# Optimization experiments

Measured on AMD Instinct MI355X. Metric: run time of the kernel, lower is better.

The kernel has to match this reference:

```python
import jax, jax.numpy as jnp
import numpy as np

C = 256
C8 = C // 8
B, D, H, W = 2, 16, 64, 64


def setup_inputs() -> dict:
    key = jax.random.key(0)
    ks = jax.random.split(key, 8)
    s = 0.05
    return {
        "x1": jax.random.normal(ks[0], (B, C, D, H, W), dtype=jnp.float32),
        "x2": jax.random.normal(ks[1], (B, C, D, H, W), dtype=jnp.float32),
        "Wq": jax.random.normal(ks[2], (C8, C), dtype=jnp.float32) * s,
        "bq": jax.random.normal(ks[3], (C8,), dtype=jnp.float32) * s,
        "Wk": jax.random.normal(ks[4], (C8, C), dtype=jnp.float32) * s,
        "bk": jax.random.normal(ks[5], (C8,), dtype=jnp.float32) * s,
        "Wv": jax.random.normal(ks[6], (C, C), dtype=jnp.float32) * s,
        "bv": jax.random.normal(ks[7], (C,), dtype=jnp.float32) * s,
    }


def _conv1x1(x, Wt, b):
    # 1x1x1 Conv3d == channel-mixing linear: x [B,Cin,D,H,W], Wt [Cout,Cin]
    return jnp.einsum('bcdhw,oc->bodhw', x, Wt) + b[None, :, None, None, None]


def reference(x1, x2, Wq, bq, Wk, bk, Wv, bv):
    q = _conv1x1(x1, Wq, bq)   # [B,C8,D,H,W]
    k = _conv1x1(x2, Wk, bk)   # [B,C8,D,H,W]
    v = _conv1x1(x2, Wv, bv)   # [B,C, D,H,W]
    # Non-softmax bilinear attention over the W axis, batched over (b,d,h)
    attn = jnp.einsum('bcdhx,bcdhy->bdhxy', q, k)        # [B,D,H,W,W]
    out = jnp.einsum('bdhxy,bcdhy->bcdhx', attn, v)      # [B,C,D,H,W]
    return out
```

## Files before the change

kernel.cpp:

```cpp
#include <hip/hip_runtime.h>

#define NB   2
#define ND   16
#define NH   64
#define DHW  65536
#define HW   4096
#define CDHW 16777216

typedef __attribute__((ext_vector_type(4))) float f32x4;
typedef __attribute__((ext_vector_type(8))) short bf16x8;
typedef unsigned short ushort_t;

#define MFMA16(a, b, c) __builtin_amdgcn_mfma_f32_16x16x32_bf16((a), (b), (c), 0, 0, 0)

#define WS_WQH 0
#define WS_WQL 8192
#define WS_WKH 16384
#define WS_WKL 24576
#define WS_WVH 32768
#define WS_WVL 98304
#define WS_WEIGHT_USHORTS 163840
#define WS_AH  (WS_WEIGHT_USHORTS)
#define WS_AL  (WS_AH + 8388608)
#define WS_FULL_BYTES ((size_t)(WS_WEIGHT_USHORTS + 16777216) * 2)

__device__ __forceinline__ void split_val(float f, short& h, short& l) {
  unsigned int u = __builtin_bit_cast(unsigned int, f);
  h = (short)(unsigned short)(u >> 16);
  float fh = __builtin_bit_cast(float, u & 0xffff0000u);
  float r = f - fh;
  l = (short)(unsigned short)(__builtin_bit_cast(unsigned int, r) >> 16);
}

__device__ __forceinline__ void load_split8(const float* __restrict__ p, bf16x8& h8, bf16x8& l8) {
  float4 a = *(const float4*)p;
  float4 b = *(const float4*)(p + 4);
  float f[8] = {a.x, a.y, a.z, a.w, b.x, b.y, b.z, b.w};
#pragma unroll
  for (int j = 0; j < 8; ++j) {
    short hh, ll;
    split_val(f[j], hh, ll);
    h8[j] = hh; l8[j] = ll;
  }
}

__device__ __forceinline__ int swzb(int row, int colb) {
  return row * 128 + (((colb) & ~15) ^ ((row & 7) << 4)) + ((colb) & 15);
}

__global__ void prep_w(const float* __restrict__ Wq, const float* __restrict__ Wk,
                       const float* __restrict__ Wv, ushort_t* __restrict__ ws) {
  int idx = blockIdx.x * 256 + threadIdx.x;
  const float* src; int off; ushort_t *H, *L;
  if (idx < 8192)       { src = Wq; off = idx;         H = ws + WS_WQH; L = ws + WS_WQL; }
  else if (idx < 16384) { src = Wk; off = idx - 8192;  H = ws + WS_WKH; L = ws + WS_WKL; }
  else if (idx < 81920) { src = Wv; off = idx - 16384; H = ws + WS_WVH; L = ws + WS_WVL; }
  else return;
  short h, l;
  split_val(src[off], h, l);
  H[off] = (ushort_t)h;
  L[off] = (ushort_t)l;
}

__global__ __launch_bounds__(256, 2) void qk_kernel(
    const float* __restrict__ x1, const float* __restrict__ x2,
    const float* __restrict__ bq, const float* __restrict__ bk,
    ushort_t* __restrict__ ws)
{
  __shared__ char qsmem[32768];
  const int tid  = threadIdx.x;
  const int lane = tid & 63;
  const int wv   = tid >> 6;
  const int l15  = lane & 15;
  const int g    = lane >> 4;

  const int grp = blockIdx.x * 4 + wv;
  const int b   = grp >> 10;
  const int rem = grp & 1023;
  const int d   = rem >> 6;
  const int h   = rem & 63;
  const size_t base = (size_t)b * CDHW + (size_t)d * HW + (size_t)h * 64;
  const float* x1p = x1 + base;
  const float* x2p = x2 + base;

  float* buf = (float*)(qsmem + wv * 8192);

  const ushort_t* WqH = ws + WS_WQH;
  const ushort_t* WqL = ws + WS_WQL;
  const ushort_t* WkH = ws + WS_WKH;
  const ushort_t* WkL = ws + WS_WKL;

  f32x4 qacc[2][4], kacc[2][4];
#pragma unroll
  for (int mt = 0; mt < 2; ++mt) {
    int r0 = mt * 16 + 4 * g;
    f32x4 bqv = (f32x4){bq[r0], bq[r0 + 1], bq[r0 + 2], bq[r0 + 3]};
    f32x4 bkv = (f32x4){bk[r0], bk[r0 + 1], bk[r0 + 2], bk[r0 + 3]};
#pragma unroll
    for (int nt = 0; nt < 4; ++nt) { qacc[mt][nt] = bqv; kacc[mt][nt] = bkv; }
  }

  const int rrow = (lane >> 4);
  const int rcol = (lane & 15) * 4;

  float4 rfA[8], rfB[8];
  auto loadc = [&](float4* rf, int i) {
    const float* src = (i < 8 ? x1p : x2p) + (size_t)(32 * (i & 7)) * DHW;
#pragma unroll
    for (int k = 0; k < 8; ++k)
      rf[k] = *(const float4*)(src + (size_t)(4 * k + rrow) * DHW + rcol);
  };
  auto writec = [&](const float4* rf) {
#pragma unroll
    for (int k = 0; k < 8; ++k)
      *(float4*)&buf[(4 * k + rrow) * 64 + rcol] = rf[k];
  };
  auto compute = [&](int i, f32x4 (&acc)[2][4], const ushort_t* Wh, const ushort_t* Wl) {
    const int kg0 = 32 * (i & 7) + 8 * g;
    bf16x8 wh0 = *(const bf16x8*)&Wh[(size_t)(l15) * 256 + kg0];
    bf16x8 wl0 = *(const bf16x8*)&Wl[(size_t)(l15) * 256 + kg0];
    bf16x8 wh1 = *(const bf16x8*)&Wh[(size_t)(16 + l15) * 256 + kg0];
    bf16x8 wl1 = *(const bf16x8*)&Wl[(size_t)(16 + l15) * 256 + kg0];
    bf16x8 bh[4], bl[4];
#pragma unroll
    for (int nt = 0; nt < 4; ++nt) {
#pragma unroll
      for (int j = 0; j < 8; ++j) {
        float f = buf[(8 * g + j) * 64 + nt * 16 + l15];
        short hh, ll;
        split_val(f, hh, ll);
        bh[nt][j] = hh; bl[nt][j] = ll;
      }
    }
#pragma unroll
    for (int nt = 0; nt < 4; ++nt) {
      acc[0][nt] = MFMA16(wh0, bh[nt], acc[0][nt]);
      acc[0][nt] = MFMA16(wh0, bl[nt], acc[0][nt]);
      acc[0][nt] = MFMA16(wl0, bh[nt], acc[0][nt]);
      acc[1][nt] = MFMA16(wh1, bh[nt], acc[1][nt]);
      acc[1][nt] = MFMA16(wh1, bl[nt], acc[1][nt]);
      acc[1][nt] = MFMA16(wl1, bh[nt], acc[1][nt]);
    }
  };

  loadc(rfA, 0);
#pragma unroll
  for (int i2 = 0; i2 < 8; ++i2) {
    const int i0 = 2 * i2, i1 = 2 * i2 + 1;
    loadc(rfB, i1);
    writec(rfA);
    if (i0 < 8) compute(i0, qacc, WqH, WqL); else compute(i0, kacc, WkH, WkL);
    if (i1 + 1 < 16) loadc(rfA, i1 + 1);
    writec(rfB);
    if (i1 < 8) compute(i1, qacc, WqH, WqL); else compute(i1, kacc, WkH, WkL);
  }

  ushort_t* ex = (ushort_t*)buf;
#pragma unroll
  for (int mt = 0; mt < 2; ++mt)
#pragma unroll
    for (int nt = 0; nt < 4; ++nt)
#pragma unroll
      for (int r = 0; r < 4; ++r) {
        short hh, ll;
        split_val(qacc[mt][nt][r], hh, ll);
        int x = nt * 16 + l15;
        ex[x * 32 + mt * 16 + 4 * g + r]        = (ushort_t)hh;
        ex[2048 + x * 32 + mt * 16 + 4 * g + r] = (ushort_t)ll;
      }
  bf16x8 qh8[4], ql8[4];
#pragma unroll
  for (int mt = 0; mt < 4; ++mt) {
    qh8[mt] = *(const bf16x8*)&ex[(mt * 16 + l15) * 32 + 8 * g];
    ql8[mt] = *(const bf16x8*)&ex[2048 + (mt * 16 + l15) * 32 + 8 * g];
  }
#pragma unroll
  for (int mt = 0; mt < 2; ++mt)
#pragma unroll
    for (int nt = 0; nt < 4; ++nt)
#pragma unroll
      for (int r = 0; r < 4; ++r) {
        short hh, ll;
        split_val(kacc[mt][nt][r], hh, ll);
        int y = nt * 16 + l15;
        ex[y * 32 + mt * 16 + 4 * g + r]        = (ushort_t)hh;
        ex[2048 + y * 32 + mt * 16 + 4 * g + r] = (ushort_t)ll;
      }
  bf16x8 kh8[4], kl8[4];
#pragma unroll
  for (int nt = 0; nt < 4; ++nt) {
    kh8[nt] = *(const bf16x8*)&ex[(nt * 16 + l15) * 32 + 8 * g];
    kl8[nt] = *(const bf16x8*)&ex[2048 + (nt * 16 + l15) * 32 + 8 * g];
  }
  f32x4 aacc[4][4];
#pragma unroll
  for (int mt = 0; mt < 4; ++mt)
#pragma unroll
    for (int nt = 0; nt < 4; ++nt) {
      f32x4 a = (f32x4){0.f, 0.f, 0.f, 0.f};
      a = MFMA16(qh8[mt], kh8[nt], a);
      a = MFMA16(qh8[mt], kl8[nt], a);
      a = MFMA16(ql8[mt], kh8[nt], a);
      aacc[mt][nt] = a;
    }
  ushort_t* Ah = ws + WS_AH + (size_t)grp * 4096;
  ushort_t* Al = ws + WS_AL + (size_t)grp * 4096;
#pragma unroll
  for (int mt = 0; mt < 4; ++mt)
#pragma unroll
    for (int nt = 0; nt < 4; ++nt)
#pragma unroll
      for (int r = 0; r < 4; ++r) {
        short hh, ll;
        split_val(aacc[mt][nt][r], hh, ll);
        int x = mt * 16 + 4 * g + r, y = nt * 16 + l15;
        Ah[x * 64 + y] = (ushort_t)hh;
        Al[x * 64 + y] = (ushort_t)ll;
      }
}

#define B_OFF_XTH  0
#define B_OFF_XTL  8192
#define B_OFF_AH   16384
#define B_OFF_AL   24576
#define B_OFF_XLIN 32768
#define B_SMEM     49152

__global__ __launch_bounds__(256, 3) void xattn_v3(
    const float* __restrict__ x2, const float* __restrict__ bv,
    const ushort_t* __restrict__ wsp, float* __restrict__ out)
{
  __shared__ char smem[B_SMEM];
  char*  XthB = smem + B_OFF_XTH;
  char*  XtlB = smem + B_OFF_XTL;
  char*  AhL  = smem + B_OFF_AH;
  char*  AlL  = smem + B_OFF_AL;
  float* Xlin = (float*)(smem + B_OFF_XLIN);

  const int tid  = threadIdx.x;
  const int lane = tid & 63;
  const int wv   = tid >> 6;
  const int l15  = lane & 15;
  const int g    = lane >> 4;

  const int bid   = blockIdx.x;
  const int grp   = bid >> 1;
  const int chalf = bid & 1;
  const int cbase = chalf * 128;
  const int b   = grp >> 10;
  const int rem = grp & 1023;
  const int d   = rem >> 6;
  const int h   = rem & 63;
  const size_t base = (size_t)b * CDHW + (size_t)d * HW + (size_t)h * 64;
  const float* x2p = x2 + base;

  const ushort_t* WvH = wsp + WS_WVH;
  const ushort_t* WvL = wsp + WS_WVL;
  const ushort_t* AhW = wsp + WS_AH + (size_t)grp * 4096;
  const ushort_t* AlW = wsp + WS_AL + (size_t)grp * 4096;

  float4 pf[4];
  auto issue_pf = [&](const float* __restrict__ src) {
#pragma unroll
    for (int i = 0; i < 4; ++i) {
      int ch = 16 * wv + g + 4 * i;
      pf[i] = *(const float4*)(src + (size_t)ch * DHW + 4 * l15);
    }
  };
  auto write_xlin = [&]() {
#pragma unroll
    for (int i = 0; i < 4; ++i) {
      int ch = 16 * wv + g + 4 * i;
      *(float4*)&Xlin[ch * 64 + 4 * l15] = pf[i];
    }
  };
  auto passB = [&]() {
#pragma unroll
    for (int bb = 0; bb < 2; ++bb) {
      int c0 = 16 * wv + 8 * bb;
      bf16x8 h8, l8;
#pragma unroll
      for (int j = 0; j < 8; ++j) {
        float f = Xlin[(c0 + j) * 64 + lane];
        short hh, ll;
        split_val(f, hh, ll);
        h8[j] = hh; l8[j] = ll;
      }
      *(bf16x8*)(XthB + swzb(lane, c0 * 2)) = h8;
      *(bf16x8*)(XtlB + swzb(lane, c0 * 2)) = l8;
    }
  };
  auto ldsx = [&](const char* B, int row, int ko) -> bf16x8 {
    return *(const bf16x8*)(B + swzb(row, ko * 2));
  };

  f32x4 vacc[2][4];
#pragma unroll
  for (int mt = 0; mt < 2; ++mt) {
    int r0 = cbase + 32 * wv + mt * 16 + 4 * g;
    f32x4 bb = (f32x4){bv[r0], bv[r0 + 1], bv[r0 + 2], bv[r0 + 3]};
#pragma unroll
    for (int nt = 0; nt < 4; ++nt) vacc[mt][nt] = bb;
  }

  issue_pf(x2p);
  {
#pragma unroll
    for (int rr = 0; rr < 2; ++rr) {
      int idx = tid + rr * 256;
      int row = idx >> 3;
      int seg = idx & 7;
      bf16x8 vh = *(const bf16x8*)&AhW[row * 64 + seg * 8];
      bf16x8 vl = *(const bf16x8*)&AlW[row * 64 + seg * 8];
      *(bf16x8*)(AhL + swzb(row, seg * 16)) = vh;
      *(bf16x8*)(AlL + swzb(row, seg * 16)) = vl;
    }
  }
  write_xlin();
  __syncthreads();

  for (int t = 0; t < 4; ++t) {
    bf16x8 w_h[2][2], w_l[2][2];
#pragma unroll
    for (int ks = 0; ks < 2; ++ks) {
      const int kg = t * 64 + ks * 32 + 8 * g;
#pragma unroll
      for (int mt = 0; mt < 2; ++mt) {
        w_h[ks][mt] = *(const bf16x8*)&WvH[(size_t)(cbase + 32 * wv + mt * 16 + l15) * 256 + kg];
        w_l[ks][mt] = *(const bf16x8*)&WvL[(size_t)(cbase + 32 * wv + mt * 16 + l15) * 256 + kg];
      }
    }
    passB();
    __syncthreads();
    if (t < 3) issue_pf(x2p + (size_t)(t + 1) * 64 * DHW);
#pragma unroll
    for (int ks = 0; ks < 2; ++ks) {
      const int ko = ks * 32 + 8 * g;
      bf16x8 xh[4], xl[4];
#pragma unroll
      for (int nt = 0; nt < 4; ++nt) {
        xh[nt] = ldsx(XthB, nt * 16 + l15, ko);
        xl[nt] = ldsx(XtlB, nt * 16 + l15, ko);
      }
      __builtin_amdgcn_s_setprio(1);
#pragma unroll
      for (int mt = 0; mt < 2; ++mt) {
#pragma unroll
        for (int nt = 0; nt < 4; ++nt) {
          vacc[mt][nt] = MFMA16(w_h[ks][mt], xh[nt], vacc[mt][nt]);
          vacc[mt][nt] = MFMA16(w_h[ks][mt], xl[nt], vacc[mt][nt]);
          vacc[mt][nt] = MFMA16(w_l[ks][mt], xh[nt], vacc[mt][nt]);
        }
      }
      __builtin_amdgcn_s_setprio(0);
    }
    if (t < 3) write_xlin();
    __syncthreads();
  }

  {
    char* VhB = smem + B_OFF_XLIN + wv * 4096;
    char* VlB = VhB + 2048;
#pragma unroll
    for (int mt = 0; mt < 2; ++mt) {
#pragma unroll
      for (int nt = 0; nt < 4; ++nt)
#pragma unroll
        for (int r = 0; r < 4; ++r) {
          short hh, ll;
          split_val(vacc[mt][nt][r], hh, ll);
          int colb = (nt * 16 + l15) * 2;
          *(ushort_t*)(VhB + swzb(4 * g + r, colb)) = (ushort_t)hh;
          *(ushort_t*)(VlB + swzb(4 * g + r, colb)) = (ushort_t)ll;
        }
      f32x4 oacc[4];
#pragma unroll
      for (int nt = 0; nt < 4; ++nt) oacc[nt] = (f32x4){0.f, 0.f, 0.f, 0.f};
      __builtin_amdgcn_s_setprio(1);
#pragma unroll
      for (int ys = 0; ys < 2; ++ys) {
        const int yo = ys * 32 + 8 * g;
        bf16x8 vh8 = *(const bf16x8*)(VhB + swzb(l15, yo * 2));
        bf16x8 vl8 = *(const bf16x8*)(VlB + swzb(l15, yo * 2));
#pragma unroll
        for (int nt = 0; nt < 4; ++nt) {
          bf16x8 ah8 = ldsx(AhL, nt * 16 + l15, yo);
          bf16x8 al8 = ldsx(AlL, nt * 16 + l15, yo);
          oacc[nt] = MFMA16(vh8, ah8, oacc[nt]);
          oacc[nt] = MFMA16(vh8, al8, oacc[nt]);
          oacc[nt] = MFMA16(vl8, ah8, oacc[nt]);
        }
      }
      __builtin_amdgcn_s_setprio(0);
#pragma unroll
      for (int nt = 0; nt < 4; ++nt)
#pragma unroll
        for (int r = 0; r < 4; ++r)
          out[base + (size_t)(cbase + 32 * wv + mt * 16 + 4 * g + r) * DHW + nt * 16 + l15] = oacc[nt][r];
    }
  }
}

#define XT_LD 72
#define QK_LD 40
#define A_LD  72
#define VB_LD 72
#define F_OFF_XTH 0
#define F_OFF_XTL 9216
#define F_OFF_R2  18432
#define F_OFF_KH  18432
#define F_OFF_KL  23552
#define F_OFF_AH  0
#define F_OFF_AL  9216
#define F_OFF_QH  36864
#define F_OFF_QL  41984
#define F_SMEM 47104

__global__ __launch_bounds__(256, 3) void xattn_fallback(
    const float* __restrict__ x1, const float* __restrict__ x2,
    const float* __restrict__ Wq, const float* __restrict__ bq,
    const float* __restrict__ Wk, const float* __restrict__ bk,
    const float* __restrict__ Wv, const float* __restrict__ bv,
    float* __restrict__ out)
{
  __shared__ char smem[F_SMEM];
  ushort_t* Xth  = (ushort_t*)(smem + F_OFF_XTH);
  ushort_t* Xtl  = (ushort_t*)(smem + F_OFF_XTL);
  float*    Xlin = (float*)(smem + F_OFF_R2);
  ushort_t* Kh   = (ushort_t*)(smem + F_OFF_KH);
  ushort_t* Kl   = (ushort_t*)(smem + F_OFF_KL);
  ushort_t* Vb   = (ushort_t*)(smem + F_OFF_R2);
  ushort_t* Ah   = (ushort_t*)(smem + F_OFF_AH);
  ushort_t* Al   = (ushort_t*)(smem + F_OFF_AL);
  ushort_t* Qh   = (ushort_t*)(smem + F_OFF_QH);
  ushort_t* Ql   = (ushort_t*)(smem + F_OFF_QL);

  const int tid  = threadIdx.x;
  const int lane = tid & 63;
  const int wv   = tid >> 6;
  const int l15  = lane & 15;
  const int g    = lane >> 4;

  const int grp = blockIdx.x;
  const int b   = grp >> 10;
  const int rem = grp & 1023;
  const int d   = rem >> 6;
  const int h   = rem & 63;
  const size_t base = (size_t)b * CDHW + (size_t)d * HW + (size_t)h * 64;

  auto passA = [&](const float* __restrict__ src) {
#pragma unroll
    for (int i = 0; i < 4; ++i) {
      int ch = 16 * wv + (lane >> 4) + 4 * i;
      int c4 = (lane & 15) << 2;
      float4 v = *(const float4*)(src + (size_t)ch * DHW + c4);
      *(float4*)&Xlin[ch * 66 + c4] = v;
    }
  };
  auto passB = [&]() {
#pragma unroll
    for (int bb = 0; bb < 2; ++bb) {
      int c0 = 16 * wv + 8 * bb;
      bf16x8 h8, l8;
#pragma unroll
      for (int j = 0; j < 8; ++j) {
        float f = Xlin[(c0 + j) * 66 + lane];
        short hh, ll;
        split_val(f, hh, ll);
        h8[j] = hh; l8[j] = ll;
      }
      *(bf16x8*)&Xth[lane * XT_LD + c0] = h8;
      *(bf16x8*)&Xtl[lane * XT_LD + c0] = l8;
    }
  };

  {
    f32x4 qacc[2];
#pragma unroll
    for (int mt = 0; mt < 2; ++mt) {
      int r0 = mt * 16 + 4 * g;
      qacc[mt] = (f32x4){bq[r0], bq[r0 + 1], bq[r0 + 2], bq[r0 + 3]};
    }
    const float* x1p = x1 + base;
    for (int t = 0; t < 4; ++t) {
      passA(x1p + (size_t)t * 64 * DHW);
      __syncthreads();
      passB();
      __syncthreads();
#pragma unroll
      for (int ks = 0; ks < 2; ++ks) {
        const int ko = ks * 32 + 8 * g;
        const int kg = t * 64 + ko;
        bf16x8 bh = *(const bf16x8*)&Xth[(16 * wv + l15) * XT_LD + ko];
        bf16x8 bl = *(const bf16x8*)&Xtl[(16 * wv + l15) * XT_LD + ko];
#pragma unroll
        for (int mt = 0; mt < 2; ++mt) {
          bf16x8 wh, wl;
          load_split8(Wq + (size_t)(mt * 16 + l15) * 256 + kg, wh, wl);
          qacc[mt] = MFMA16(wh, bh, qacc[mt]);
          qacc[mt] = MFMA16(wh, bl, qacc[mt]);
          qacc[mt] = MFMA16(wl, bh, qacc[mt]);
        }
      }
      __syncthreads();
    }
    const int x = 16 * wv + l15;
#pragma unroll
    for (int mt = 0; mt < 2; ++mt)
#pragma unroll
      for (int r = 0; r < 4; ++r) {
        short hh, ll;
        split_val(qacc[mt][r], hh, ll);
        Qh[x * QK_LD + mt * 16 + 4 * g + r] = (ushort_t)hh;
        Ql[x * QK_LD + mt * 16 + 4 * g + r] = (ushort_t)ll;
      }
  }

  f32x4 vacc[4][4];
  {
    f32x4 kacc[2];
#pragma unroll
    for (int mt = 0; mt < 2; ++mt) {
      int r0 = mt * 16 + 4 * g;
      kacc[mt] = (f32x4){bk[r0], bk[r0 + 1], bk[r0 + 2], bk[r0 + 3]};
    }
#pragma unroll
    for (int mt = 0; mt < 4; ++mt) {
      int r0 = 64 * wv + mt * 16 + 4 * g;
      f32x4 bb = (f32x4){bv[r0], bv[r0 + 1], bv[r0 + 2], bv[r0 + 3]};
#pragma unroll
      for (int nt = 0; nt < 4; ++nt) vacc[mt][nt] = bb;
    }
    const float* x2p = x2 + base;
    for (int t = 0; t < 4; ++t) {
      passA(x2p + (size_t)t * 64 * DHW);
      __syncthreads();
      passB();
      __syncthreads();
#pragma unroll
      for (int ks = 0; ks < 2; ++ks) {
        const int ko = ks * 32 + 8 * g;
        const int kg = t * 64 + ko;
        bf16x8 xh[4], xl[4];
#pragma unroll
        for (int nt = 0; nt < 4; ++nt) {
          xh[nt] = *(const bf16x8*)&Xth[(nt * 16 + l15) * XT_LD + ko];
          xl[nt] = *(const bf16x8*)&Xtl[(nt * 16 + l15) * XT_LD + ko];
        }
        {
          bf16x8 bh = *(const bf16x8*)&Xth[(16 * wv + l15) * XT_LD + ko];
          bf16x8 bl = *(const bf16x8*)&Xtl[(16 * wv + l15) * XT_LD + ko];
#pragma unroll
          for (int mt = 0; mt < 2; ++mt) {
            bf16x8 wh, wl;
            load_split8(Wk + (size_t)(mt * 16 + l15) * 256 + kg, wh, wl);
            kacc[mt] = MFMA16(wh, bh, kacc[mt]);
            kacc[mt] = MFMA16(wh, bl, kacc[mt]);
            kacc[mt] = MFMA16(wl, bh, kacc[mt]);
          }
        }
#pragma unroll
        for (int mt = 0; mt < 4; ++mt) {
          bf16x8 wh, wl;
          load_split8(Wv + (size_t)(64 * wv + mt * 16 + l15) * 256 + kg, wh, wl);
#pragma unroll
          for (int nt = 0; nt < 4; ++nt) {
            vacc[mt][nt] = MFMA16(wh, xh[nt], vacc[mt][nt]);
            vacc[mt][nt] = MFMA16(wh, xl[nt], vacc[mt][nt]);
            vacc[mt][nt] = MFMA16(wl, xh[nt], vacc[mt][nt]);
          }
        }
      }
      __syncthreads();
    }
    const int y = 16 * wv + l15;
#pragma unroll
    for (int mt = 0; mt < 2; ++mt)
#pragma unroll
      for (int r = 0; r < 4; ++r) {
        short hh, ll;
        split_val(kacc[mt][r], hh, ll);
        Kh[y * QK_LD + mt * 16 + 4 * g + r] = (ushort_t)hh;
        Kl[y * QK_LD + mt * 16 + 4 * g + r] = (ushort_t)ll;
      }
  }
  __syncthreads();

  {
    const int y = 16 * wv + l15;
    bf16x8 kh = *(const bf16x8*)&Kh[y * QK_LD + 8 * g];
    bf16x8 kl = *(const bf16x8*)&Kl[y * QK_LD + 8 * g];
    f32x4 acc[4];
#pragma unroll
    for (int mt = 0; mt < 4; ++mt) acc[mt] = (f32x4){0.f, 0.f, 0.f, 0.f};
#pragma unroll
    for (int mt = 0; mt < 4; ++mt) {
      bf16x8 qh = *(const bf16x8*)&Qh[(mt * 16 + l15) * QK_LD + 8 * g];
      bf16x8 ql = *(const bf16x8*)&Ql[(mt * 16 + l15) * QK_LD + 8 * g];
      acc[mt] = MFMA16(qh, kh, acc[mt]);
      acc[mt] = MFMA16(qh, kl, acc[mt]);
      acc[mt] = MFMA16(ql, kh, acc[mt]);
    }
#pragma unroll
    for (int mt = 0; mt < 4; ++mt)
#pragma unroll
      for (int r = 0; r < 4; ++r) {
        short hh, ll;
        split_val(acc[mt][r], hh, ll);
        Ah[(mt * 16 + 4 * g + r) * A_LD + y] = (ushort_t)hh;
        Al[(mt * 16 + 4 * g + r) * A_LD + y] = (ushort_t)ll;
      }
  }
  __syncthreads();

  {
    ushort_t* Vh = Vb + wv * 2304;
    ushort_t* Vl = Vh + 1152;
    const int cb = 64 * wv;
#pragma unroll
    for (int mt = 0; mt < 4; ++mt) {
#pragma unroll
      for (int nt = 0; nt < 4; ++nt)
#pragma unroll
        for (int r = 0; r < 4; ++r) {
          short hh, ll;
          split_val(vacc[mt][nt][r], hh, ll);
          Vh[(4 * g + r) * VB_LD + nt * 16 + l15] = (ushort_t)hh;
          Vl[(4 * g + r) * VB_LD + nt * 16 + l15] = (ushort_t)ll;
        }
      f32x4 oacc[4];
#pragma unroll
      for (int nt = 0; nt < 4; ++nt) oacc[nt] = (f32x4){0.f, 0.f, 0.f, 0.f};
#pragma unroll
      for (int ys = 0; ys < 2; ++ys) {
        const int yo = ys * 32 + 8 * g;
        bf16x8 vh8 = *(const bf16x8*)&Vh[l15 * VB_LD + yo];
        bf16x8 vl8 = *(const bf16x8*)&Vl[l15 * VB_LD + yo];
#pragma unroll
        for (int nt = 0; nt < 4; ++nt) {
          bf16x8 ah8 = *(const bf16x8*)&Ah[(nt * 16 + l15) * A_LD + yo];
          bf16x8 al8 = *(const bf16x8*)&Al[(nt * 16 + l15) * A_LD + yo];
          oacc[nt] = MFMA16(vh8, ah8, oacc[nt]);
          oacc[nt] = MFMA16(vh8, al8, oacc[nt]);
          oacc[nt] = MFMA16(vl8, ah8, oacc[nt]);
        }
      }
#pragma unroll
      for (int nt = 0; nt < 4; ++nt)
#pragma unroll
        for (int r = 0; r < 4; ++r)
          out[base + (size_t)(cb + mt * 16 + 4 * g + r) * DHW + nt * 16 + l15] = oacc[nt][r];
    }
  }
}

extern "C" void kernel_launch(void* const* d_in, const int* in_sizes, int n_in,
                              void* d_out, int out_size, void* d_ws, size_t ws_size,
                              hipStream_t stream)
{
  const float* x1 = (const float*)d_in[0];
  const float* x2 = (const float*)d_in[1];
  const float* Wq = (const float*)d_in[2];
  const float* bq = (const float*)d_in[3];
  const float* Wk = (const float*)d_in[4];
  const float* bk = (const float*)d_in[5];
  const float* Wv = (const float*)d_in[6];
  const float* bv = (const float*)d_in[7];
  float* out = (float*)d_out;

  if (d_ws && ws_size >= WS_FULL_BYTES) {
    ushort_t* ws = (ushort_t*)d_ws;
    hipLaunchKernelGGL(prep_w, dim3(320), dim3(256), 0, stream, Wq, Wk, Wv, ws);
    hipLaunchKernelGGL(qk_kernel, dim3(512), dim3(256), 0, stream, x1, x2, bq, bk, ws);
    hipLaunchKernelGGL(xattn_v3, dim3(4096), dim3(256), 0, stream, x2, bv, ws, out);
  } else {
    hipLaunchKernelGGL(xattn_fallback, dim3(NB * ND * NH), dim3(256), 0, stream,
                       x1, x2, Wq, bq, Wk, bk, Wv, bv, out);
  }
}
```

Measured before the change: 214.4 us.

## Merge channel halves per block, use direct global-to-LDS loads, double-buffer weights

Each block now computes all 256 output channels of one (b,d,h) row instead of splitting them across two blocks, so the x2 row is read and bf16-split once rather than twice and the grid is halved. The x2 tile is staged through global_load_lds straight into shared memory, replacing the register prefetch and LDS write. Wv fragments are software-pipelined in two register buffers across the k-substeps. The cost is roughly double the accumulator registers per wave (16 f32x4 tiles) under launch bounds of 3 blocks, which risks spills or lower occupancy.

```diff
diff --git a/kernel.cpp b/kernel.cpp
--- a/kernel.cpp
+++ b/kernel.cpp
@@ -23,6 +23,10 @@
 #define WS_AH  (WS_WEIGHT_USHORTS)
 #define WS_AL  (WS_AH + 8388608)
 #define WS_FULL_BYTES ((size_t)(WS_WEIGHT_USHORTS + 16777216) * 2)
+
+#define GLOAD16(gp, lp) \
+  __builtin_amdgcn_global_load_lds((const __attribute__((address_space(1))) void*)(const void*)(gp), \
+                                   (__attribute__((address_space(3))) void*)(void*)(lp), 16, 0, 0)
 
 __device__ __forceinline__ void split_val(float f, short& h, short& l) {
   unsigned int u = __builtin_bit_cast(unsigned int, f);
@@ -226,7 +230,7 @@
 #define B_OFF_XLIN 32768
 #define B_SMEM     49152
 
-__global__ __launch_bounds__(256, 3) void xattn_v3(
+__global__ __launch_bounds__(256, 3) void xattn_v4(
     const float* __restrict__ x2, const float* __restrict__ bv,
     const ushort_t* __restrict__ wsp, float* __restrict__ out)
 {
@@ -243,10 +247,7 @@
   const int l15  = lane & 15;
   const int g    = lane >> 4;
 
-  const int bid   = blockIdx.x;
-  const int grp   = bid >> 1;
-  const int chalf = bid & 1;
-  const int cbase = chalf * 128;
+  const int grp = blockIdx.x;
   const int b   = grp >> 10;
   const int rem = grp & 1023;
   const int d   = rem >> 6;
@@ -259,19 +260,12 @@
   const ushort_t* AhW = wsp + WS_AH + (size_t)grp * 4096;
   const ushort_t* AlW = wsp + WS_AL + (size_t)grp * 4096;
 
-  float4 pf[4];
-  auto issue_pf = [&](const float* __restrict__ src) {
+  auto stage_x = [&](const float* __restrict__ src) {
 #pragma unroll
     for (int i = 0; i < 4; ++i) {
-      int ch = 16 * wv + g + 4 * i;
-      pf[i] = *(const float4*)(src + (size_t)ch * DHW + 4 * l15);
-    }
-  };
-  auto write_xlin = [&]() {
-#pragma unroll
-    for (int i = 0; i < 4; ++i) {
-      int ch = 16 * wv + g + 4 * i;
-      *(float4*)&Xlin[ch * 64 + 4 * l15] = pf[i];
+      const float* gp = src + (size_t)(16 * wv + g + 4 * i) * DHW + 4 * l15;
+      char* lp = (char*)Xlin + (size_t)(16 * wv + 4 * i) * 256;
+      GLOAD16(gp, lp);
     }
   };
   auto passB = [&]() {
@@ -293,17 +287,25 @@
   auto ldsx = [&](const char* B, int row, int ko) -> bf16x8 {
     return *(const bf16x8*)(B + swzb(row, ko * 2));
   };
-
-  f32x4 vacc[2][4];
-#pragma unroll
-  for (int mt = 0; mt < 2; ++mt) {
-    int r0 = cbase + 32 * wv + mt * 16 + 4 * g;
+  auto loadw = [&](bf16x8 (&wh)[4], bf16x8 (&wl)[4], int t, int ks) {
+    const int kg = t * 64 + ks * 32 + 8 * g;
+#pragma unroll
+    for (int mt = 0; mt < 4; ++mt) {
+      wh[mt] = *(const bf16x8*)&WvH[(size_t)(64 * wv + mt * 16 + l15) * 256 + kg];
+      wl[mt] = *(const bf16x8*)&WvL[(size_t)(64 * wv + mt * 16 + l15) * 256 + kg];
+    }
+  };
+
+  f32x4 vacc[4][4];
+#pragma unroll
+  for (int mt = 0; mt < 4; ++mt) {
+    int r0 = 64 * wv + mt * 16 + 4 * g;
     f32x4 bb = (f32x4){bv[r0], bv[r0 + 1], bv[r0 + 2], bv[r0 + 3]};
 #pragma unroll
     for (int nt = 0; nt < 4; ++nt) vacc[mt][nt] = bb;
   }
 
-  issue_pf(x2p);
+  stage_x(x2p);
   {
 #pragma unroll
     for (int rr = 0; rr < 2; ++rr) {
@@ -316,26 +318,17 @@
       *(bf16x8*)(AlL + swzb(row, seg * 16)) = vl;
     }
   }
-  write_xlin();
+  bf16x8 wAh[4], wAl[4], wBh[4], wBl[4];
+  loadw(wAh, wAl, 0, 0);
   __syncthreads();
 
   for (int t = 0; t < 4; ++t) {
-    bf16x8 w_h[2][2], w_l[2][2];
-#pragma unroll
-    for (int ks = 0; ks < 2; ++ks) {
-      const int kg = t * 64 + ks * 32 + 8 * g;
-#pragma unroll
-      for (int mt = 0; mt < 2; ++mt) {
-        w_h[ks][mt] = *(const bf16x8*)&WvH[(size_t)(cbase + 32 * wv + mt * 16 + l15) * 256 + kg];
-        w_l[ks][mt] = *(const bf16x8*)&WvL[(size_t)(cbase + 32 * wv + mt * 16 + l15) * 256 + kg];
-      }
-    }
     passB();
     __syncthreads();
-    if (t < 3) issue_pf(x2p + (size_t)(t + 1) * 64 * DHW);
-#pragma unroll
-    for (int ks = 0; ks < 2; ++ks) {
-      const int ko = ks * 32 + 8 * g;
+    if (t < 3) stage_x(x2p + (size_t)(t + 1) * 64 * DHW);
+    loadw(wBh, wBl, t, 1);
+    {
+      const int ko = 8 * g;
       bf16x8 xh[4], xl[4];
 #pragma unroll
       for (int nt = 0; nt < 4; ++nt) {
@@ -344,25 +337,44 @@
       }
       __builtin_amdgcn_s_setprio(1);
 #pragma unroll
-      for (int mt = 0; mt < 2; ++mt) {
+      for (int mt = 0; mt < 4; ++mt)
 #pragma unroll
         for (int nt = 0; nt < 4; ++nt) {
-          vacc[mt][nt] = MFMA16(w_h[ks][mt], xh[nt], vacc[mt][nt]);
-          vacc[mt][nt] = MFMA16(w_h[ks][mt], xl[nt], vacc[mt][nt]);
-          vacc[mt][nt] = MFMA16(w_l[ks][mt], xh[nt], vacc[mt][nt]);
-        }
-      }
+          vacc[mt][nt] = MFMA16(wAh[mt], xh[nt], vacc[mt][nt]);
+          vacc[mt][nt] = MFMA16(wAh[mt], xl[nt], vacc[mt][nt]);
+          vacc[mt][nt] = MFMA16(wAl[mt], xh[nt], vacc[mt][nt]);
+        }
       __builtin_amdgcn_s_setprio(0);
     }
-    if (t < 3) write_xlin();
+    if (t < 3) loadw(wAh, wAl, t + 1, 0);
+    {
+      const int ko = 32 + 8 * g;
+      bf16x8 xh[4], xl[4];
+#pragma unroll
+      for (int nt = 0; nt < 4; ++nt) {
+        xh[nt] = ldsx(XthB, nt * 16 + l15, ko);
+        xl[nt] = ldsx(XtlB, nt * 16 + l15, ko);
+      }
+      __builtin_amdgcn_s_setprio(1);
+#pragma unroll
+      for (int mt = 0; mt < 4; ++mt)
+#pragma unroll
+        for (int nt = 0; nt < 4; ++nt) {
+          vacc[mt][nt] = MFMA16(wBh[mt], xh[nt], vacc[mt][nt]);
+          vacc[mt][nt] = MFMA16(wBh[mt], xl[nt], vacc[mt][nt]);
+          vacc[mt][nt] = MFMA16(wBl[mt], xh[nt], vacc[mt][nt]);
+        }
+      __builtin_amdgcn_s_setprio(0);
+    }
     __syncthreads();
   }
 
   {
     char* VhB = smem + B_OFF_XLIN + wv * 4096;
     char* VlB = VhB + 2048;
-#pragma unroll
-    for (int mt = 0; mt < 2; ++mt) {
+    const int cb = 64 * wv;
+#pragma unroll
+    for (int mt = 0; mt < 4; ++mt) {
 #pragma unroll
       for (int nt = 0; nt < 4; ++nt)
 #pragma unroll
@@ -396,7 +408,7 @@
       for (int nt = 0; nt < 4; ++nt)
 #pragma unroll
         for (int r = 0; r < 4; ++r)
-          out[base + (size_t)(cbase + 32 * wv + mt * 16 + 4 * g + r) * DHW + nt * 16 + l15] = oacc[nt][r];
+          out[base + (size_t)(cb + mt * 16 + 4 * g + r) * DHW + nt * 16 + l15] = oacc[nt][r];
     }
   }
 }
@@ -672,7 +684,7 @@
     ushort_t* ws = (ushort_t*)d_ws;
     hipLaunchKernelGGL(prep_w, dim3(320), dim3(256), 0, stream, Wq, Wk, Wv, ws);
     hipLaunchKernelGGL(qk_kernel, dim3(512), dim3(256), 0, stream, x1, x2, bq, bk, ws);
-    hipLaunchKernelGGL(xattn_v3, dim3(4096), dim3(256), 0, stream, x2, bv, ws, out);
+    hipLaunchKernelGGL(xattn_v4, dim3(NB * ND * NH), dim3(256), 0, stream, x2, bv, ws, out);
   } else {
     hipLaunchKernelGGL(xattn_fallback, dim3(NB * ND * NH), dim3(256), 0, stream,
                        x1, x2, Wq, bq, Wk, bk, Wv, bv, out);
```

After: 264.8 us. 1.23x slower.
